# Kernel optimization log

Hardware: AMD Instinct MI355X
Metric: run time of the kernel (lower is better)

## Reference

```python
import jax, jax.numpy as jnp
import numpy as np

N_NODES = 50000
N_EDGES = 800000
IN_CH = 256
OUT_CH = 64  # heads=1
NEG_SLOPE = 0.2


def setup_inputs() -> dict:
    key = jax.random.key(0)
    k1, k2, k3, k4, k5 = jax.random.split(key, 5)
    x = jax.random.normal(k1, (N_NODES, IN_CH), dtype=jnp.float32)
    edge_index = jax.random.randint(k2, (2, N_EDGES), 0, N_NODES, dtype=jnp.int64)
    # glorot init for dense weight [out, in] (torch Linear layout) and att [out, 2]
    s_w = np.sqrt(6.0 / (OUT_CH + IN_CH)).astype(np.float32)
    W = jax.random.uniform(k3, (OUT_CH, IN_CH), minval=-s_w, maxval=s_w, dtype=jnp.float32)
    b = jnp.zeros((OUT_CH,), dtype=jnp.float32)
    s_a = np.sqrt(6.0 / (OUT_CH + 2)).astype(np.float32)
    att = jax.random.uniform(k4, (OUT_CH, 2), minval=-s_a, maxval=s_a, dtype=jnp.float32)
    return {"x": x, "edge_index": edge_index, "W": W, "b": b, "att": att}


def reference(x, edge_index, W, b, att):
    n = x.shape[0]
    # dense projection: feature [N, OUT_CH]
    feature = x @ W.T + b
    # per-node attention contributions: e_pre [N, 2]
    e_pre = feature @ att
    tar = edge_index[0]  # flow='target_to_source'
    src = edge_index[1]
    # edge logit = leakyrelu(a_tar(t) + a_src(s)); self-loop logit per node
    logit_edge = jax.nn.leaky_relu(e_pre[tar, 0] + e_pre[src, 1], NEG_SLOPE)
    logit_self = jax.nn.leaky_relu(e_pre[:, 0] + e_pre[:, 1], NEG_SLOPE)
    # segment softmax over {self edge} U {incoming edges} per target node
    m = jnp.maximum(jax.ops.segment_max(logit_edge, tar, num_segments=n), logit_self)
    exp_edge = jnp.exp(logit_edge - m[tar])
    exp_self = jnp.exp(logit_self - m)
    denom = exp_self + jax.ops.segment_sum(exp_edge, tar, num_segments=n)
    alpha = exp_edge / denom[tar]          # [E]
    alpha_self = exp_self / denom          # [N]
    # weighted gather-scatter aggregation (fused_gas_agg)
    msgs = alpha[:, None] * feature[src]   # [E, OUT_CH]
    out = alpha_self[:, None] * feature + jax.ops.segment_sum(msgs, tar, num_segments=n)
    return out
```

## Files before the change

### kernel.cpp

```cpp
#include <hip/hip_runtime.h>
#include <math.h>

#define N_NODES 50000
#define N_EDGES 800000
#define IN_CH 256
#define OUT_CH 64
#define NEG_SLOPE 0.2f
#define PAD 64
#define DEGS 16

#define EDGE_BLOCKS 196
#define GEMM_BLOCKS 782

typedef __bf16 bf16x4 __attribute__((ext_vector_type(4)));
typedef __bf16 bf16x8 __attribute__((ext_vector_type(8)));
typedef float  f32x4  __attribute__((ext_vector_type(4)));

__global__ __launch_bounds__(256) void k_zero(int* __restrict__ deg)
{
    int idx = (blockIdx.x * 256 + threadIdx.x) * 4;
    if (idx + 4 <= N_NODES * DEGS)
        *reinterpret_cast<int4*>(&deg[idx]) = make_int4(0, 0, 0, 0);
}

__global__ __launch_bounds__(256) void k_fused(
    const float* __restrict__ x, const float* __restrict__ W,
    const float* __restrict__ bias, const float* __restrict__ att,
    const int* __restrict__ ei,
    __bf16* __restrict__ featb, float* __restrict__ e0,
    float* __restrict__ e1, int* __restrict__ deg,
    unsigned short* __restrict__ pcsr)
{
    __shared__ __bf16 B[64][264];

    const int t = threadIdx.x;

    if (blockIdx.x < EDGE_BLOCKS) {
        const int base = blockIdx.x * 4096 + t * 4;
        int tn[16], sn[16], sl[16];
        #pragma unroll
        for (int c = 0; c < 4; ++c) {
            int e = base + c * 1024;
            if (e + 4 <= N_EDGES) {
                *reinterpret_cast<int4*>(&tn[c * 4]) =
                    *reinterpret_cast<const int4*>(&ei[e]);
                *reinterpret_cast<int4*>(&sn[c * 4]) =
                    *reinterpret_cast<const int4*>(&ei[N_EDGES + e]);
            } else {
                #pragma unroll
                for (int j = 0; j < 4; ++j) {
                    int ee = e + j;
                    tn[c * 4 + j] = (ee < N_EDGES) ? ei[ee] : -1;
                    sn[c * 4 + j] = (ee < N_EDGES) ? ei[N_EDGES + ee] : 0;
                }
            }
        }
        #pragma unroll
        for (int k = 0; k < 16; ++k)
            sl[k] = (tn[k] >= 0) ? atomicAdd(&deg[tn[k] * DEGS], 1) : 0x7fffffff;
        #pragma unroll
        for (int k = 0; k < 16; ++k)
            if (tn[k] >= 0 && sl[k] < PAD)
                pcsr[(size_t)tn[k] * PAD + sl[k]] = (unsigned short)sn[k];
        return;
    }

    const int row0 = (blockIdx.x - EDGE_BLOCKS) * 64;
    const int wv   = t >> 6;
    const int li   = t & 63;
    const int lm   = li & 15;
    const int lq   = li >> 4;

    {
        const int sr = t >> 2;
        const int cq = t & 3;
        #pragma unroll
        for (int j = 0; j < 4; ++j) {
            #pragma unroll
            for (int i = 0; i < 4; ++i) {
                int kk = j * 64 + cq * 16 + i * 4;
                float4 w1 = *reinterpret_cast<const float4*>(&W[(size_t)sr * IN_CH + kk]);
                bf16x4 g = {(__bf16)w1.x, (__bf16)w1.y, (__bf16)w1.z, (__bf16)w1.w};
                *reinterpret_cast<bf16x4*>(&B[sr][kk]) = g;
            }
        }
    }
    __syncthreads();

    const int myrow = row0 + wv * 16 + lm;
    const float* xrow = x + (size_t)(myrow < N_NODES ? myrow : 0) * IN_CH;

    f32x4 acc[4];
    #pragma unroll
    for (int tn = 0; tn < 4; ++tn) acc[tn] = (f32x4){0.f, 0.f, 0.f, 0.f};

    #pragma unroll
    for (int kb = 0; kb < 8; ++kb) {
        int ko = kb * 32 + lq * 8;
        float4 a0 = *reinterpret_cast<const float4*>(&xrow[ko]);
        float4 a1 = *reinterpret_cast<const float4*>(&xrow[ko + 4]);
        bf16x8 a = {(__bf16)a0.x, (__bf16)a0.y, (__bf16)a0.z, (__bf16)a0.w,
                    (__bf16)a1.x, (__bf16)a1.y, (__bf16)a1.z, (__bf16)a1.w};
        #pragma unroll
        for (int tn = 0; tn < 4; ++tn) {
            bf16x8 b = *reinterpret_cast<const bf16x8*>(&B[tn * 16 + lm][ko]);
            acc[tn] = __builtin_amdgcn_mfma_f32_16x16x32_bf16(a, b, acc[tn], 0, 0, 0);
        }
    }

    float att0[4], att1[4], bv[4];
    #pragma unroll
    for (int tn = 0; tn < 4; ++tn) {
        int c = tn * 16 + lm;
        att0[tn] = att[c * 2 + 0];
        att1[tn] = att[c * 2 + 1];
        bv[tn]   = bias[c];
    }

    float p0[4] = {0.f, 0.f, 0.f, 0.f};
    float p1[4] = {0.f, 0.f, 0.f, 0.f};
    #pragma unroll
    for (int r = 0; r < 4; ++r) {
        int row = row0 + wv * 16 + lq * 4 + r;
        #pragma unroll
        for (int tn = 0; tn < 4; ++tn) {
            float f = acc[tn][r] + bv[tn];
            if (row < N_NODES)
                featb[(size_t)row * OUT_CH + tn * 16 + lm] = (__bf16)f;
            p0[r] += f * att0[tn];
            p1[r] += f * att1[tn];
        }
    }

    #pragma unroll
    for (int m = 1; m < 16; m <<= 1) {
        #pragma unroll
        for (int r = 0; r < 4; ++r) {
            p0[r] += __shfl_xor(p0[r], m, 64);
            p1[r] += __shfl_xor(p1[r], m, 64);
        }
    }
    if (lm == 0) {
        #pragma unroll
        for (int r = 0; r < 4; ++r) {
            int row = row0 + wv * 16 + lq * 4 + r;
            if (row < N_NODES) {
                e0[row] = p0[r];
                e1[row] = p1[r];
            }
        }
    }
}

__global__ __launch_bounds__(256) void k_gather(
    const float* __restrict__ e0, const float* __restrict__ e1,
    const __bf16* __restrict__ featb, const int* __restrict__ deg,
    const unsigned short* __restrict__ pcsr, float* __restrict__ out)
{
    int t    = blockIdx.x * 4 + (threadIdx.x >> 6);
    int lane = threadIdx.x & 63;
    if (t >= N_NODES) return;

    const int g  = lane >> 4;
    const int cl = lane & 15;

    int cnt = deg[t * DEGS];
    cnt = cnt > PAD ? PAD : cnt;

    float e0t = e0[t];

    int si = (int)pcsr[(size_t)t * PAD + lane];
    si = (lane < cnt) ? si : 0;
    float qi = e1[si];
    float zi = e0t + qi;
    float wi = (lane < cnt) ? __expf(zi > 0.f ? zi : NEG_SLOPE * zi) : 0.f;

    float zs  = e0t + e1[t];
    float wsf = __expf(zs > 0.f ? zs : NEG_SLOPE * zs);
    bf16x4 sf = *reinterpret_cast<const bf16x4*>(&featb[(size_t)t * OUT_CH + cl * 4]);

    float wsum = wi;
    #pragma unroll
    for (int m = 1; m < 64; m <<= 1)
        wsum += __shfl_xor(wsum, m, 64);
    wsum += wsf;

    f32x4 acc = {0.f, 0.f, 0.f, 0.f};
    for (int i = 0; i < cnt; i += 16) {
        int   s0 = __shfl(si, i + g,      64);
        int   s1 = __shfl(si, i + 4 + g,  64);
        int   s2 = __shfl(si, i + 8 + g,  64);
        int   s3 = __shfl(si, i + 12 + g, 64);
        float w0 = __shfl(wi, i + g,      64);
        float w1 = __shfl(wi, i + 4 + g,  64);
        float w2 = __shfl(wi, i + 8 + g,  64);
        float w3 = __shfl(wi, i + 12 + g, 64);
        bf16x4 f0 = *reinterpret_cast<const bf16x4*>(&featb[(size_t)s0 * OUT_CH + cl * 4]);
        bf16x4 f1 = *reinterpret_cast<const bf16x4*>(&featb[(size_t)s1 * OUT_CH + cl * 4]);
        bf16x4 f2 = *reinterpret_cast<const bf16x4*>(&featb[(size_t)s2 * OUT_CH + cl * 4]);
        bf16x4 f3 = *reinterpret_cast<const bf16x4*>(&featb[(size_t)s3 * OUT_CH + cl * 4]);
        #pragma unroll
        for (int j = 0; j < 4; ++j)
            acc[j] += w0 * (float)f0[j] + w1 * (float)f1[j]
                    + w2 * (float)f2[j] + w3 * (float)f3[j];
    }

    #pragma unroll
    for (int j = 0; j < 4; ++j) {
        acc[j] += __shfl_xor(acc[j], 16, 64);
        acc[j] += __shfl_xor(acc[j], 32, 64);
    }

    if (g == 0) {
        float inv = 1.f / wsum;
        float4 o;
        o.x = (acc[0] + wsf * (float)sf[0]) * inv;
        o.y = (acc[1] + wsf * (float)sf[1]) * inv;
        o.z = (acc[2] + wsf * (float)sf[2]) * inv;
        o.w = (acc[3] + wsf * (float)sf[3]) * inv;
        *reinterpret_cast<float4*>(&out[(size_t)t * OUT_CH + cl * 4]) = o;
    }
}

extern "C" void kernel_launch(void* const* d_in, const int* in_sizes, int n_in,
                              void* d_out, int out_size, void* d_ws, size_t ws_size,
                              hipStream_t stream)
{
    const float* x    = (const float*)d_in[0];
    const int*   ei   = (const int*)d_in[1];
    const float* W    = (const float*)d_in[2];
    const float* bias = (const float*)d_in[3];
    const float* att  = (const float*)d_in[4];
    float* out = (float*)d_out;

    __bf16* featb = (__bf16*)d_ws;
    float*  e0    = (float*)(featb + (size_t)N_NODES * OUT_CH);
    float*  e1    = e0 + N_NODES;
    int*    deg   = (int*)(e1 + N_NODES);
    unsigned short* pcsr = (unsigned short*)(deg + (size_t)N_NODES * DEGS);

    dim3 blk(256);

    k_zero<<<dim3((N_NODES * DEGS / 4 + 255) / 256), blk, 0, stream>>>(deg);

    k_fused<<<dim3(EDGE_BLOCKS + GEMM_BLOCKS), blk, 0, stream>>>(
        x, W, bias, att, ei, featb, e0, e1, deg, pcsr);

    k_gather<<<dim3((N_NODES + 3) / 4), blk, 0, stream>>>(
        e0, e1, featb, deg, pcsr, out);
}
```

Measured before the change: 161.5 us.

## Use sentinel-filled padded CSR to drop degree load and prefetch first neighbor batch

```diff
diff --git a/kernel.cpp b/kernel.cpp
--- a/kernel.cpp
+++ b/kernel.cpp
@@ -16,11 +16,19 @@
 typedef __bf16 bf16x8 __attribute__((ext_vector_type(8)));
 typedef float  f32x4  __attribute__((ext_vector_type(4)));
 
-__global__ __launch_bounds__(256) void k_zero(int* __restrict__ deg)
-{
-    int idx = (blockIdx.x * 256 + threadIdx.x) * 4;
-    if (idx + 4 <= N_NODES * DEGS)
-        *reinterpret_cast<int4*>(&deg[idx]) = make_int4(0, 0, 0, 0);
+__global__ __launch_bounds__(256) void k_zero(int* __restrict__ deg,
+                                              unsigned short* __restrict__ pcsr)
+{
+    const int tid    = blockIdx.x * 256 + threadIdx.x;
+    const int stride = gridDim.x * 256;
+
+    for (int i = tid; i < N_NODES * DEGS / 4; i += stride)
+        *reinterpret_cast<int4*>(&deg[i * 4]) = make_int4(0, 0, 0, 0);
+
+    int4* p4 = reinterpret_cast<int4*>(pcsr);
+    const int np = N_NODES * PAD / 8;
+    for (int i = tid; i < np; i += stride)
+        p4[i] = make_int4(-1, -1, -1, -1);
 }
 
 __global__ __launch_bounds__(256) void k_fused(
@@ -154,7 +162,7 @@
 
 __global__ __launch_bounds__(256) void k_gather(
     const float* __restrict__ e0, const float* __restrict__ e1,
-    const __bf16* __restrict__ featb, const int* __restrict__ deg,
+    const __bf16* __restrict__ featb,
     const unsigned short* __restrict__ pcsr, float* __restrict__ out)
 {
     int t    = blockIdx.x * 4 + (threadIdx.x >> 6);
@@ -164,20 +172,36 @@
     const int g  = lane >> 4;
     const int cl = lane & 15;
 
-    int cnt = deg[t * DEGS];
-    cnt = cnt > PAD ? PAD : cnt;
-
     float e0t = e0[t];
 
-    int si = (int)pcsr[(size_t)t * PAD + lane];
-    si = (lane < cnt) ? si : 0;
+    unsigned short raw = 0xFFFFu;
+    if (lane < 32) raw = pcsr[(size_t)t * PAD + lane];
+    unsigned long long bm = __ballot(raw != 0xFFFFu);
+    int cnt = __popcll(bm);
+    if (cnt == 32) {
+        if (lane >= 32) raw = pcsr[(size_t)t * PAD + lane];
+        bm  = __ballot(raw != 0xFFFFu);
+        cnt = __popcll(bm);
+    }
+    const bool valid = (raw != 0xFFFFu);
+    int si = valid ? (int)raw : 0;
+
+    int s0 = __shfl(si, 0 + g,  64);
+    int s1 = __shfl(si, 4 + g,  64);
+    int s2 = __shfl(si, 8 + g,  64);
+    int s3 = __shfl(si, 12 + g, 64);
+    bf16x4 f0 = *reinterpret_cast<const bf16x4*>(&featb[(size_t)s0 * OUT_CH + cl * 4]);
+    bf16x4 f1 = *reinterpret_cast<const bf16x4*>(&featb[(size_t)s1 * OUT_CH + cl * 4]);
+    bf16x4 f2 = *reinterpret_cast<const bf16x4*>(&featb[(size_t)s2 * OUT_CH + cl * 4]);
+    bf16x4 f3 = *reinterpret_cast<const bf16x4*>(&featb[(size_t)s3 * OUT_CH + cl * 4]);
+    bf16x4 sf = *reinterpret_cast<const bf16x4*>(&featb[(size_t)t  * OUT_CH + cl * 4]);
+
     float qi = e1[si];
     float zi = e0t + qi;
-    float wi = (lane < cnt) ? __expf(zi > 0.f ? zi : NEG_SLOPE * zi) : 0.f;
+    float wi = valid ? __expf(zi > 0.f ? zi : NEG_SLOPE * zi) : 0.f;
 
     float zs  = e0t + e1[t];
     float wsf = __expf(zs > 0.f ? zs : NEG_SLOPE * zs);
-    bf16x4 sf = *reinterpret_cast<const bf16x4*>(&featb[(size_t)t * OUT_CH + cl * 4]);
 
     float wsum = wi;
     #pragma unroll
@@ -185,24 +209,33 @@
         wsum += __shfl_xor(wsum, m, 64);
     wsum += wsf;
 
-    f32x4 acc = {0.f, 0.f, 0.f, 0.f};
-    for (int i = 0; i < cnt; i += 16) {
-        int   s0 = __shfl(si, i + g,      64);
-        int   s1 = __shfl(si, i + 4 + g,  64);
-        int   s2 = __shfl(si, i + 8 + g,  64);
-        int   s3 = __shfl(si, i + 12 + g, 64);
-        float w0 = __shfl(wi, i + g,      64);
-        float w1 = __shfl(wi, i + 4 + g,  64);
-        float w2 = __shfl(wi, i + 8 + g,  64);
-        float w3 = __shfl(wi, i + 12 + g, 64);
-        bf16x4 f0 = *reinterpret_cast<const bf16x4*>(&featb[(size_t)s0 * OUT_CH + cl * 4]);
-        bf16x4 f1 = *reinterpret_cast<const bf16x4*>(&featb[(size_t)s1 * OUT_CH + cl * 4]);
-        bf16x4 f2 = *reinterpret_cast<const bf16x4*>(&featb[(size_t)s2 * OUT_CH + cl * 4]);
-        bf16x4 f3 = *reinterpret_cast<const bf16x4*>(&featb[(size_t)s3 * OUT_CH + cl * 4]);
+    float w0 = __shfl(wi, 0 + g,  64);
+    float w1 = __shfl(wi, 4 + g,  64);
+    float w2 = __shfl(wi, 8 + g,  64);
+    float w3 = __shfl(wi, 12 + g, 64);
+    f32x4 acc;
+    #pragma unroll
+    for (int j = 0; j < 4; ++j)
+        acc[j] = w0 * (float)f0[j] + w1 * (float)f1[j]
+               + w2 * (float)f2[j] + w3 * (float)f3[j];
+
+    for (int i = 16; i < cnt; i += 16) {
+        int   t0 = __shfl(si, i + g,      64);
+        int   t1 = __shfl(si, i + 4 + g,  64);
+        int   t2 = __shfl(si, i + 8 + g,  64);
+        int   t3 = __shfl(si, i + 12 + g, 64);
+        float v0 = __shfl(wi, i + g,      64);
+        float v1 = __shfl(wi, i + 4 + g,  64);
+        float v2 = __shfl(wi, i + 8 + g,  64);
+        float v3 = __shfl(wi, i + 12 + g, 64);
+        bf16x4 h0 = *reinterpret_cast<const bf16x4*>(&featb[(size_t)t0 * OUT_CH + cl * 4]);
+        bf16x4 h1 = *reinterpret_cast<const bf16x4*>(&featb[(size_t)t1 * OUT_CH + cl * 4]);
+        bf16x4 h2 = *reinterpret_cast<const bf16x4*>(&featb[(size_t)t2 * OUT_CH + cl * 4]);
+        bf16x4 h3 = *reinterpret_cast<const bf16x4*>(&featb[(size_t)t3 * OUT_CH + cl * 4]);
         #pragma unroll
         for (int j = 0; j < 4; ++j)
-            acc[j] += w0 * (float)f0[j] + w1 * (float)f1[j]
-                    + w2 * (float)f2[j] + w3 * (float)f3[j];
+            acc[j] += v0 * (float)h0[j] + v1 * (float)h1[j]
+                    + v2 * (float)h2[j] + v3 * (float)h3[j];
     }
 
     #pragma unroll
@@ -241,11 +274,11 @@
 
     dim3 blk(256);
 
-    k_zero<<<dim3((N_NODES * DEGS / 4 + 255) / 256), blk, 0, stream>>>(deg);
+    k_zero<<<dim3(2048), blk, 0, stream>>>(deg, pcsr);
 
     k_fused<<<dim3(EDGE_BLOCKS + GEMM_BLOCKS), blk, 0, stream>>>(
         x, W, bias, att, ei, featb, e0, e1, deg, pcsr);
 
     k_gather<<<dim3((N_NODES + 3) / 4), blk, 0, stream>>>(
-        e0, e1, featb, deg, pcsr, out);
-}
+        e0, e1, featb, pcsr, out);
+}
```

Measured after the change: 162.4 us. About the same (+0.6%).
